# Optimization experiments

Hardware: AMD Instinct MI355X
Metric: run time of the kernel (lower is better)

The kernel has to match this reference:

```python
import jax, jax.numpy as jnp
import numpy as np

B, L, D = 4, 2048, 1024
H, KD, VD = 16, 64, 64
EPS = 1e-5


def setup_inputs() -> dict:
    key = jax.random.key(0)
    ks = jax.random.split(key, 12)
    s_in = 1.0 / np.sqrt(D)
    s_out = 1.0 / np.sqrt(H * VD)
    return {
        "queries": jax.random.normal(ks[0], (B, L, D), dtype=jnp.float32),
        "Wq": jax.random.uniform(ks[1], (D, H * KD), jnp.float32, -s_in, s_in),
        "bq": jax.random.uniform(ks[2], (H * KD,), jnp.float32, -s_in, s_in),
        "Wk": jax.random.uniform(ks[3], (D, H * KD), jnp.float32, -s_in, s_in),
        "bk": jax.random.uniform(ks[4], (H * KD,), jnp.float32, -s_in, s_in),
        "Wv": jax.random.uniform(ks[5], (D, H * VD), jnp.float32, -s_in, s_in),
        "bv": jax.random.uniform(ks[6], (H * VD,), jnp.float32, -s_in, s_in),
        "Wo": jax.random.uniform(ks[7], (H * VD, D), jnp.float32, -s_out, s_out),
        "bo": jax.random.uniform(ks[8], (D,), jnp.float32, -s_out, s_out),
        "gamma": jnp.ones((D,), jnp.float32),
        "beta": jnp.zeros((D,), jnp.float32),
    }


def reference(queries, Wq, bq, Wk, bk, Wv, bv, Wo, bo, gamma, beta):
    # QKV projections -> [B, L, H, head_dim]
    q = (queries @ Wq + bq).reshape(B, L, H, KD)
    k = (queries @ Wk + bk).reshape(B, L, H, KD)
    v = (queries @ Wv + bv).reshape(B, L, H, VD)
    # scaled dot-product attention per head: scores [B, H, Lq, Lk]
    scores = jnp.einsum("bqhd,bkhd->bhqk", q, k) / np.sqrt(KD).astype(np.float32)
    attn = jax.nn.softmax(scores, axis=-1)
    out = jnp.einsum("bhqk,bkhd->bqhd", attn, v).reshape(B, L, H * VD)
    # out projection (dropout is identity in eval), residual + LayerNorm
    res = out @ Wo + bo + queries
    mu = jnp.mean(res, axis=-1, keepdims=True)
    var = jnp.var(res, axis=-1, keepdims=True)
    return (res - mu) / jnp.sqrt(var + EPS) * gamma + beta
```

## Files before the change

### kernel.cpp

```cpp
#include <hip/hip_runtime.h>
#include <hip/hip_bf16.h>

#define BATCH 4
#define SEQ   2048
#define DIM   1024
#define NHEAD 16
#define HDIM  64
#define EPS_LN 1e-5f
#define QSCALE 0.18033688011112042f

typedef __attribute__((ext_vector_type(8))) short short8;
typedef __attribute__((ext_vector_type(4))) float f32x4;
typedef __attribute__((ext_vector_type(4))) unsigned uint32x4;

__device__ __forceinline__ unsigned short f2bf(float x) {
    __hip_bfloat16 h = __float2bfloat16(x);
    return *reinterpret_cast<unsigned short*>(&h);
}
__device__ __forceinline__ unsigned int pack2bf(float a, float b) {
    __hip_bfloat162 h = __float22bfloat162_rn(float2{a, b});
    return *reinterpret_cast<unsigned int*>(&h);
}

__device__ __forceinline__ void pl32_swap(unsigned& a, unsigned& b) {
    asm("v_permlane32_swap_b32 %0, %1" : "+v"(a), "+v"(b));
}
__device__ __forceinline__ void pl16_swap(unsigned& a, unsigned& b) {
    asm("v_permlane16_swap_b32 %0, %1" : "+v"(a), "+v"(b));
}

__device__ __forceinline__ void gl_lds16(const void* g, void* l) {
    __builtin_amdgcn_global_load_lds(
        (const __attribute__((address_space(1))) unsigned int*)g,
        (__attribute__((address_space(3))) unsigned int*)l,
        16, 0, 0);
}

__global__ __launch_bounds__(256) void prep_kernel(const float* __restrict__ W0,
                                                   const float* __restrict__ W1,
                                                   const float* __restrict__ W2,
                                                   const float* __restrict__ W3,
                                                   const float* __restrict__ queries,
                                                   unsigned short* __restrict__ Wqkvt,
                                                   unsigned short* __restrict__ Wot,
                                                   unsigned short* __restrict__ qout)
{
    const int z = blockIdx.z;
    const int t = threadIdx.x;

    if (z == 4) {
        const int nthr = 16 * 16 * 256;
        int i = (blockIdx.y * 16 + blockIdx.x) * 256 + t;
        for (int it = 0; it < (BATCH * SEQ * DIM / 4) / nthr; it++, i += nthr) {
            float4 v = ((const float4*)queries)[i];
            ushort4 u;
            u.x = f2bf(v.x); u.y = f2bf(v.y); u.z = f2bf(v.z); u.w = f2bf(v.w);
            ((ushort4*)qout)[i] = u;
        }
        return;
    }

    __shared__ float Ts[64][65];
    const float* W = (z == 0) ? W0 : (z == 1) ? W1 : (z == 2) ? W2 : W3;
    unsigned short* Wt = (z == 3) ? Wot : (Wqkvt + (size_t)z * DIM * DIM);

    const int k0 = blockIdx.y * 64, n0 = blockIdx.x * 64;
    const int lr = t >> 2, lq = t & 3;

#pragma unroll
    for (int i = 0; i < 4; i++) {
        float4 v = *(const float4*)(W + (size_t)(k0 + lr) * DIM + n0 + (lq * 4 + i) * 4);
        Ts[lr][(lq * 4 + i) * 4 + 0] = v.x;
        Ts[lr][(lq * 4 + i) * 4 + 1] = v.y;
        Ts[lr][(lq * 4 + i) * 4 + 2] = v.z;
        Ts[lr][(lq * 4 + i) * 4 + 3] = v.w;
    }
    __syncthreads();
#pragma unroll
    for (int i = 0; i < 4; i++) {
        const int c = lq * 16 + i * 4;
        ushort4 u;
        u.x = f2bf(Ts[c + 0][lr]);
        u.y = f2bf(Ts[c + 1][lr]);
        u.z = f2bf(Ts[c + 2][lr]);
        u.w = f2bf(Ts[c + 3][lr]);
        *(ushort4*)(Wt + (size_t)(n0 + lr) * DIM + k0 + c) = u;
    }
}

__global__ __launch_bounds__(256) void gemm_qkv(const unsigned short* __restrict__ A,
                                                const unsigned short* __restrict__ Bt,
                                                const float* __restrict__ bq,
                                                const float* __restrict__ bk,
                                                const float* __restrict__ bv,
                                                unsigned short* __restrict__ Qbf,
                                                unsigned short* __restrict__ Kbf,
                                                unsigned short* __restrict__ Vtb)
{
    __shared__ __attribute__((aligned(16))) unsigned short As[128 * 32];
    __shared__ __attribute__((aligned(16))) unsigned short Bs[128 * 32];

    const int tid = threadIdx.x;
    const int w = tid >> 6, lane = tid & 63;
    const int col = lane & 15, quad = lane >> 4;
    const int wm = (w >> 1) * 64, wn = (w & 1) * 64;
    const int m0 = blockIdx.y * 128, n0 = blockIdx.x * 128;

    f32x4 acc[4][4] = {};
    const int srow = tid >> 2, sc4 = tid & 3;

    for (int k0 = 0; k0 < DIM; k0 += 32) {
        __syncthreads();
#pragma unroll
        for (int it = 0; it < 2; it++) {
            gl_lds16(A  + (size_t)(m0 + srow + it * 64) * DIM + k0 + sc4 * 8,
                     (char*)As + w * 1024 + it * 4096);
            gl_lds16(Bt + (size_t)(n0 + srow + it * 64) * DIM + k0 + sc4 * 8,
                     (char*)Bs + w * 1024 + it * 4096);
        }
        __syncthreads();

        short8 af[4], bf[4];
#pragma unroll
        for (int mt = 0; mt < 4; mt++) af[mt] = *(short8*)&As[(wm + mt * 16 + col) * 32 + quad * 8];
#pragma unroll
        for (int nt = 0; nt < 4; nt++) bf[nt] = *(short8*)&Bs[(wn + nt * 16 + col) * 32 + quad * 8];

#pragma unroll
        for (int mt = 0; mt < 4; mt++)
#pragma unroll
            for (int nt = 0; nt < 4; nt++)
                acc[mt][nt] = __builtin_amdgcn_mfma_f32_16x16x32_bf16(af[mt], bf[nt], acc[mt][nt], 0, 0, 0);
    }

    const int sector = n0 >> 10;
    const float* bias = (sector == 0) ? bq : (sector == 1) ? bk : bv;

#pragma unroll
    for (int nt = 0; nt < 4; nt++) {
        const int n = n0 + wn + nt * 16 + col;
        const int nloc = n - (sector << 10);
        const float bvv = bias[nloc];
#pragma unroll
        for (int mt = 0; mt < 4; mt++) {
            const int mbase = m0 + wm + mt * 16 + quad * 4;
            if (sector == 0) {
#pragma unroll
                for (int r = 0; r < 4; r++)
                    Qbf[(size_t)(mbase + r) * DIM + nloc] = f2bf((acc[mt][nt][r] + bvv) * QSCALE);
            } else if (sector == 1) {
#pragma unroll
                for (int r = 0; r < 4; r++)
                    Kbf[(size_t)(mbase + r) * DIM + nloc] = f2bf(acc[mt][nt][r] + bvv);
            } else {
                const int h = nloc >> 6, d = nloc & 63;
                const int b = mbase >> 11, l = mbase & 2047;
                ushort4 u;
                u.x = f2bf(acc[mt][nt][0] + bvv);
                u.y = f2bf(acc[mt][nt][1] + bvv);
                u.z = f2bf(acc[mt][nt][2] + bvv);
                u.w = f2bf(acc[mt][nt][3] + bvv);
                *(ushort4*)(Vtb + ((size_t)((b * NHEAD + h) * HDIM + d)) * SEQ + l) = u;
            }
        }
    }
}

__global__ __launch_bounds__(256) void gemm_out(const unsigned short* __restrict__ A,
                                                const unsigned short* __restrict__ Bt,
                                                const float* __restrict__ bias,
                                                const float* __restrict__ resid,
                                                float* __restrict__ Cout)
{
    __shared__ __attribute__((aligned(16))) unsigned short As[128 * 32];
    __shared__ __attribute__((aligned(16))) unsigned short Bs[128 * 32];

    const int tid = threadIdx.x;
    const int w = tid >> 6, lane = tid & 63;
    const int col = lane & 15, quad = lane >> 4;
    const int wm = (w >> 1) * 64, wn = (w & 1) * 64;
    const int m0 = blockIdx.y * 128, n0 = blockIdx.x * 128;

    f32x4 acc[4][4] = {};
    const int srow = tid >> 2, sc4 = tid & 3;

    for (int k0 = 0; k0 < DIM; k0 += 32) {
        __syncthreads();
#pragma unroll
        for (int it = 0; it < 2; it++) {
            gl_lds16(A  + (size_t)(m0 + srow + it * 64) * DIM + k0 + sc4 * 8,
                     (char*)As + w * 1024 + it * 4096);
            gl_lds16(Bt + (size_t)(n0 + srow + it * 64) * DIM + k0 + sc4 * 8,
                     (char*)Bs + w * 1024 + it * 4096);
        }
        __syncthreads();

        short8 af[4], bf[4];
#pragma unroll
        for (int mt = 0; mt < 4; mt++) af[mt] = *(short8*)&As[(wm + mt * 16 + col) * 32 + quad * 8];
#pragma unroll
        for (int nt = 0; nt < 4; nt++) bf[nt] = *(short8*)&Bs[(wn + nt * 16 + col) * 32 + quad * 8];

#pragma unroll
        for (int mt = 0; mt < 4; mt++)
#pragma unroll
            for (int nt = 0; nt < 4; nt++)
                acc[mt][nt] = __builtin_amdgcn_mfma_f32_16x16x32_bf16(af[mt], bf[nt], acc[mt][nt], 0, 0, 0);
    }

#pragma unroll
    for (int nt = 0; nt < 4; nt++) {
        const int n = n0 + wn + nt * 16 + col;
        const float bvv = bias[n];
#pragma unroll
        for (int mt = 0; mt < 4; mt++) {
            const int mbase = m0 + wm + mt * 16 + quad * 4;
#pragma unroll
            for (int r = 0; r < 4; r++) {
                const size_t off = (size_t)(mbase + r) * DIM + n;
                Cout[off] = acc[mt][nt][r] + bvv + resid[off];
            }
        }
    }
}

__global__ __launch_bounds__(512) void attn_mfma(const unsigned short* __restrict__ Qb,
                                                 const unsigned short* __restrict__ Kb,
                                                 const unsigned short* __restrict__ Vt,
                                                 unsigned short* __restrict__ Ob)
{
    __shared__ __attribute__((aligned(16))) unsigned short Ks[2 * 64 * 64];
    __shared__ __attribute__((aligned(16))) unsigned short Vs[2 * 64 * 64];

    const int tid = threadIdx.x;
    const int w = tid >> 6, lane = tid & 63;
    const int col = lane & 15, quad = lane >> 4;
    const int cs  = col & 7;
    const int ca  = quad ^ cs;
    const int cb  = (quad ^ 4) ^ cs;

    const int bh  = blockIdx.x & 63;
    const int qt_ = blockIdx.x >> 6;
    const int b   = bh >> 4;
    const int h   = bh & 15;

    const int q0 = qt_ * 256 + w * 32;

    short8 qf[2][2];
#pragma unroll
    for (int qt = 0; qt < 2; qt++) {
        const size_t base = ((size_t)(b * SEQ) + q0 + qt * 16 + col) * DIM + h * HDIM + quad * 8;
        qf[qt][0] = *(const short8*)(Qb + base);
        qf[qt][1] = *(const short8*)(Qb + base + 32);
    }

    short8 onesf;
    {
        const short v = (col == 0) ? (short)0x3F80 : (short)0;
        onesf = short8{v, v, v, v, v, v, v, v};
    }

    f32x4 o[4][2] = {};
    f32x4 od[2]   = {};

    const size_t kbase0 = ((size_t)(b * SEQ)) * DIM + h * HDIM;
    const size_t vbase0 = ((size_t)((b * NHEAD + h) * HDIM)) * SEQ;

    const int lr  = lane >> 3;
    const int swc = (lane & 7) ^ lr;

    {
        const int row = w * 8 + lr;
        gl_lds16(Kb + kbase0 + (size_t)row * DIM + swc * 8, (char*)Ks + w * 1024);
        gl_lds16(Vt + vbase0 + (size_t)row * SEQ + swc * 8, (char*)Vs + w * 1024);
    }
    __syncthreads();

    for (int kt = 0; kt < SEQ / 64; kt++) {
        const int cur = kt & 1, nxt = cur ^ 1;
        const unsigned short* Ksb = Ks + cur * 4096;
        const unsigned short* Vsb = Vs + cur * 4096;

        if (kt + 1 < SEQ / 64) {
            const int row = w * 8 + lr;
            gl_lds16(Kb + kbase0 + (size_t)((kt + 1) * 64 + row) * DIM + swc * 8,
                     (char*)Ks + nxt * 8192 + w * 1024);
            gl_lds16(Vt + vbase0 + (size_t)row * SEQ + (kt + 1) * 64 + swc * 8,
                     (char*)Vs + nxt * 8192 + w * 1024);
        }

        short8 pf[2][2];
#pragma unroll
        for (int f = 0; f < 2; f++) {
            short8 kfe0 = *(short8*)&Ksb[((f * 2 + 0) * 16 + col) * 64 + ca * 8];
            short8 kfe1 = *(short8*)&Ksb[((f * 2 + 0) * 16 + col) * 64 + cb * 8];
            short8 kfo0 = *(short8*)&Ksb[((f * 2 + 1) * 16 + col) * 64 + ca * 8];
            short8 kfo1 = *(short8*)&Ksb[((f * 2 + 1) * 16 + col) * 64 + cb * 8];
#pragma unroll
            for (int qt = 0; qt < 2; qt++) {
                f32x4 se = {};
                se = __builtin_amdgcn_mfma_f32_16x16x32_bf16(kfe0, qf[qt][0], se, 0, 0, 0);
                se = __builtin_amdgcn_mfma_f32_16x16x32_bf16(kfe1, qf[qt][1], se, 0, 0, 0);
                f32x4 so = {};
                so = __builtin_amdgcn_mfma_f32_16x16x32_bf16(kfo0, qf[qt][0], so, 0, 0, 0);
                so = __builtin_amdgcn_mfma_f32_16x16x32_bf16(kfo1, qf[qt][1], so, 0, 0, 0);

                unsigned a0 = pack2bf(__builtin_amdgcn_exp2f(se[0]), __builtin_amdgcn_exp2f(se[1]));
                unsigned b0 = pack2bf(__builtin_amdgcn_exp2f(se[2]), __builtin_amdgcn_exp2f(se[3]));
                unsigned a1 = pack2bf(__builtin_amdgcn_exp2f(so[0]), __builtin_amdgcn_exp2f(so[1]));
                unsigned b1 = pack2bf(__builtin_amdgcn_exp2f(so[2]), __builtin_amdgcn_exp2f(so[3]));

                pl32_swap(a0, a1);
                pl32_swap(b0, b1);
                pl16_swap(a0, a1);
                pl16_swap(b0, b1);

                uint32x4 cv = {a0, b0, a1, b1};
                pf[qt][f] = __builtin_bit_cast(short8, cv);
            }
        }

        __builtin_amdgcn_s_setprio(1);
#pragma unroll
        for (int qt = 0; qt < 2; qt++) {
            od[qt] = __builtin_amdgcn_mfma_f32_16x16x32_bf16(onesf, pf[qt][0], od[qt], 0, 0, 0);
            od[qt] = __builtin_amdgcn_mfma_f32_16x16x32_bf16(onesf, pf[qt][1], od[qt], 0, 0, 0);
        }

#pragma unroll
        for (int mt = 0; mt < 4; mt++) {
            short8 vf0 = *(short8*)&Vsb[(mt * 16 + col) * 64 + ca * 8];
            short8 vf1 = *(short8*)&Vsb[(mt * 16 + col) * 64 + cb * 8];
#pragma unroll
            for (int qt = 0; qt < 2; qt++) {
                o[mt][qt] = __builtin_amdgcn_mfma_f32_16x16x32_bf16(vf0, pf[qt][0], o[mt][qt], 0, 0, 0);
                o[mt][qt] = __builtin_amdgcn_mfma_f32_16x16x32_bf16(vf1, pf[qt][1], o[mt][qt], 0, 0, 0);
            }
        }
        __builtin_amdgcn_s_setprio(0);

        __syncthreads();
    }

#pragma unroll
    for (int qt = 0; qt < 2; qt++) {
        const float den = __shfl(od[qt][0], col);
        const float inv = 1.f / den;
        const size_t rowoff = ((size_t)(b * SEQ) + q0 + qt * 16 + col) * DIM + h * HDIM;
#pragma unroll
        for (int mt = 0; mt < 4; mt++) {
            ushort4 u;
            u.x = f2bf(o[mt][qt][0] * inv);
            u.y = f2bf(o[mt][qt][1] * inv);
            u.z = f2bf(o[mt][qt][2] * inv);
            u.w = f2bf(o[mt][qt][3] * inv);
            *(ushort4*)(Ob + rowoff + mt * 16 + quad * 4) = u;
        }
    }
}

__global__ __launch_bounds__(256) void layernorm_kernel(float* __restrict__ res,
                                                        const float* __restrict__ gamma,
                                                        const float* __restrict__ beta)
{
    const int tid = threadIdx.x;
    const int row = blockIdx.x;
    float4 xv = ((const float4*)(res + (size_t)row * DIM))[tid];

    float s  = xv.x + xv.y + xv.z + xv.w;
    float sq = xv.x * xv.x + xv.y * xv.y + xv.z * xv.z + xv.w * xv.w;
#pragma unroll
    for (int off = 32; off; off >>= 1) {
        s  += __shfl_xor(s, off);
        sq += __shfl_xor(sq, off);
    }
    __shared__ float sm[8];
    const int w = tid >> 6, lane = tid & 63;
    if (lane == 0) { sm[w] = s; sm[4 + w] = sq; }
    __syncthreads();
    const float st  = sm[0] + sm[1] + sm[2] + sm[3];
    const float sqt = sm[4] + sm[5] + sm[6] + sm[7];
    const float mu   = st * (1.f / DIM);
    const float var  = sqt * (1.f / DIM) - mu * mu;
    const float rstd = rsqrtf(var + EPS_LN);

    float4 g  = ((const float4*)gamma)[tid];
    float4 be = ((const float4*)beta)[tid];
    float4 o;
    o.x = (xv.x - mu) * rstd * g.x + be.x;
    o.y = (xv.y - mu) * rstd * g.y + be.y;
    o.z = (xv.z - mu) * rstd * g.z + be.z;
    o.w = (xv.w - mu) * rstd * g.w + be.w;
    ((float4*)(res + (size_t)row * DIM))[tid] = o;
}

extern "C" void kernel_launch(void* const* d_in, const int* in_sizes, int n_in,
                              void* d_out, int out_size, void* d_ws, size_t ws_size,
                              hipStream_t stream)
{
    const float* queries = (const float*)d_in[0];
    const float* Wq = (const float*)d_in[1];
    const float* bq = (const float*)d_in[2];
    const float* Wk = (const float*)d_in[3];
    const float* bk = (const float*)d_in[4];
    const float* Wv = (const float*)d_in[5];
    const float* bv = (const float*)d_in[6];
    const float* Wo = (const float*)d_in[7];
    const float* bo = (const float*)d_in[8];
    const float* gamma = (const float*)d_in[9];
    const float* beta  = (const float*)d_in[10];
    float* outp = (float*)d_out;

    const int M = BATCH * SEQ;
    const size_t BUF = (size_t)M * DIM;
    const size_t WSZ = (size_t)DIM * DIM;

    unsigned short* w0  = (unsigned short*)d_ws;
    unsigned short* qin = w0;
    unsigned short* Qbf = w0 + BUF;
    unsigned short* Kbf = w0 + 2 * BUF;
    unsigned short* Vtb = w0 + 3 * BUF;
    unsigned short* Wqkvt = w0 + 4 * BUF;
    unsigned short* Wot   = Wqkvt + 3 * WSZ;
    unsigned short* Obf = qin;

    dim3 blk(256);

    dim3 pgrid(DIM / 64, DIM / 64, 5);
    prep_kernel<<<pgrid, blk, 0, stream>>>(Wq, Wk, Wv, Wo, queries, Wqkvt, Wot, qin);

    dim3 qkvgrid(3 * DIM / 128, M / 128);
    gemm_qkv<<<qkvgrid, blk, 0, stream>>>(qin, Wqkvt, bq, bk, bv, Qbf, Kbf, Vtb);

    attn_mfma<<<BATCH * NHEAD * (SEQ / 256), dim3(512), 0, stream>>>(Qbf, Kbf, Vtb, Obf);

    dim3 ogrid(DIM / 128, M / 128);
    gemm_out<<<ogrid, blk, 0, stream>>>(Obf, Wot, bo, queries, outp);

    layernorm_kernel<<<M, blk, 0, stream>>>(outp, gamma, beta);
}
```

Before: 305.5 us.

## Split attention key tiles across warp pairs and reduce partial outputs in LDS

Each block now covers 128 queries instead of 256. Its 8 warps form 4 query groups × 2 key halves: each warp computes scores and P·V for half of each 64-key tile. The two partial outputs and denominators are then combined through shared memory (reusing the K/V buffers) before normalisation and the store. This doubles the grid to 1024 blocks for better CU occupancy and load balance, at the cost of twice as many K/V tile loads per query and an extra LDS reduction at the end.

New measurement: 308.1 us. No clear change (+0.8%).

```diff
diff --git a/kernel.cpp b/kernel.cpp
--- a/kernel.cpp
+++ b/kernel.cpp
@@ -231,9 +231,11 @@
 {
     __shared__ __attribute__((aligned(16))) unsigned short Ks[2 * 64 * 64];
     __shared__ __attribute__((aligned(16))) unsigned short Vs[2 * 64 * 64];
+    __shared__ float DsX[128];
 
     const int tid = threadIdx.x;
     const int w = tid >> 6, lane = tid & 63;
+    const int qw = w & 3, kw = w >> 2;
     const int col = lane & 15, quad = lane >> 4;
     const int cs  = col & 7;
     const int ca  = quad ^ cs;
@@ -244,7 +246,7 @@
     const int b   = bh >> 4;
     const int h   = bh & 15;
 
-    const int q0 = qt_ * 256 + w * 32;
+    const int q0 = qt_ * 128 + qw * 32;
 
     short8 qf[2][2];
 #pragma unroll
@@ -289,13 +291,13 @@
                      (char*)Vs + nxt * 8192 + w * 1024);
         }
 
-        short8 pf[2][2];
-#pragma unroll
-        for (int f = 0; f < 2; f++) {
-            short8 kfe0 = *(short8*)&Ksb[((f * 2 + 0) * 16 + col) * 64 + ca * 8];
-            short8 kfe1 = *(short8*)&Ksb[((f * 2 + 0) * 16 + col) * 64 + cb * 8];
-            short8 kfo0 = *(short8*)&Ksb[((f * 2 + 1) * 16 + col) * 64 + ca * 8];
-            short8 kfo1 = *(short8*)&Ksb[((f * 2 + 1) * 16 + col) * 64 + cb * 8];
+        short8 pf[2];
+        {
+            const int nte = kw * 2 + 0, nto = kw * 2 + 1;
+            short8 kfe0 = *(short8*)&Ksb[(nte * 16 + col) * 64 + ca * 8];
+            short8 kfe1 = *(short8*)&Ksb[(nte * 16 + col) * 64 + cb * 8];
+            short8 kfo0 = *(short8*)&Ksb[(nto * 16 + col) * 64 + ca * 8];
+            short8 kfo1 = *(short8*)&Ksb[(nto * 16 + col) * 64 + cb * 8];
 #pragma unroll
             for (int qt = 0; qt < 2; qt++) {
                 f32x4 se = {};
@@ -316,45 +318,57 @@
                 pl16_swap(b0, b1);
 
                 uint32x4 cv = {a0, b0, a1, b1};
-                pf[qt][f] = __builtin_bit_cast(short8, cv);
+                pf[qt] = __builtin_bit_cast(short8, cv);
             }
         }
 
         __builtin_amdgcn_s_setprio(1);
 #pragma unroll
+        for (int qt = 0; qt < 2; qt++)
+            od[qt] = __builtin_amdgcn_mfma_f32_16x16x32_bf16(onesf, pf[qt], od[qt], 0, 0, 0);
+
+#pragma unroll
+        for (int mt = 0; mt < 4; mt++) {
+            short8 vf = *(short8*)&Vsb[(mt * 16 + col) * 64 + (kw ? cb : ca) * 8];
+#pragma unroll
+            for (int qt = 0; qt < 2; qt++)
+                o[mt][qt] = __builtin_amdgcn_mfma_f32_16x16x32_bf16(vf, pf[qt], o[mt][qt], 0, 0, 0);
+        }
+        __builtin_amdgcn_s_setprio(0);
+
+        __syncthreads();
+    }
+
+    float4* xbuf = (qw & 2) ? (float4*)Vs : (float4*)Ks;
+    const int xbase = (qw & 1) * 512;
+    if (kw == 1) {
+#pragma unroll
+        for (int mt = 0; mt < 4; mt++)
+#pragma unroll
+            for (int qt = 0; qt < 2; qt++)
+                xbuf[xbase + (mt * 2 + qt) * 64 + lane] = __builtin_bit_cast(float4, o[mt][qt]);
+        if (quad == 0) {
+            DsX[(qw * 2 + 0) * 16 + col] = od[0][0];
+            DsX[(qw * 2 + 1) * 16 + col] = od[1][0];
+        }
+    }
+    __syncthreads();
+    if (kw == 0) {
+#pragma unroll
         for (int qt = 0; qt < 2; qt++) {
-            od[qt] = __builtin_amdgcn_mfma_f32_16x16x32_bf16(onesf, pf[qt][0], od[qt], 0, 0, 0);
-            od[qt] = __builtin_amdgcn_mfma_f32_16x16x32_bf16(onesf, pf[qt][1], od[qt], 0, 0, 0);
-        }
-
-#pragma unroll
-        for (int mt = 0; mt < 4; mt++) {
-            short8 vf0 = *(short8*)&Vsb[(mt * 16 + col) * 64 + ca * 8];
-            short8 vf1 = *(short8*)&Vsb[(mt * 16 + col) * 64 + cb * 8];
-#pragma unroll
-            for (int qt = 0; qt < 2; qt++) {
-                o[mt][qt] = __builtin_amdgcn_mfma_f32_16x16x32_bf16(vf0, pf[qt][0], o[mt][qt], 0, 0, 0);
-                o[mt][qt] = __builtin_amdgcn_mfma_f32_16x16x32_bf16(vf1, pf[qt][1], o[mt][qt], 0, 0, 0);
+            const float den = __shfl(od[qt][0], col) + DsX[(qw * 2 + qt) * 16 + col];
+            const float inv = 1.f / den;
+            const size_t rowoff = ((size_t)(b * SEQ) + q0 + qt * 16 + col) * DIM + h * HDIM;
+#pragma unroll
+            for (int mt = 0; mt < 4; mt++) {
+                const float4 p = xbuf[xbase + (mt * 2 + qt) * 64 + lane];
+                ushort4 u;
+                u.x = f2bf((o[mt][qt][0] + p.x) * inv);
+                u.y = f2bf((o[mt][qt][1] + p.y) * inv);
+                u.z = f2bf((o[mt][qt][2] + p.z) * inv);
+                u.w = f2bf((o[mt][qt][3] + p.w) * inv);
+                *(ushort4*)(Ob + rowoff + mt * 16 + quad * 4) = u;
             }
-        }
-        __builtin_amdgcn_s_setprio(0);
-
-        __syncthreads();
-    }
-
-#pragma unroll
-    for (int qt = 0; qt < 2; qt++) {
-        const float den = __shfl(od[qt][0], col);
-        const float inv = 1.f / den;
-        const size_t rowoff = ((size_t)(b * SEQ) + q0 + qt * 16 + col) * DIM + h * HDIM;
-#pragma unroll
-        for (int mt = 0; mt < 4; mt++) {
-            ushort4 u;
-            u.x = f2bf(o[mt][qt][0] * inv);
-            u.y = f2bf(o[mt][qt][1] * inv);
-            u.z = f2bf(o[mt][qt][2] * inv);
-            u.w = f2bf(o[mt][qt][3] * inv);
-            *(ushort4*)(Ob + rowoff + mt * 16 + quad * 4) = u;
         }
     }
 }
@@ -432,7 +446,7 @@
     dim3 qkvgrid(3 * DIM / 128, M / 128);
     gemm_qkv<<<qkvgrid, blk, 0, stream>>>(qin, Wqkvt, bq, bk, bv, Qbf, Kbf, Vtb);
 
-    attn_mfma<<<BATCH * NHEAD * (SEQ / 256), dim3(512), 0, stream>>>(Qbf, Kbf, Vtb, Obf);
+    attn_mfma<<<BATCH * NHEAD * (SEQ / 128), dim3(512), 0, stream>>>(Qbf, Kbf, Vtb, Obf);
 
     dim3 ogrid(DIM / 128, M / 128);
     gemm_out<<<ogrid, blk, 0, stream>>>(Obf, Wot, bo, queries, outp);
```

## Double KV tile to 128 keys per iteration and interleave QK and PV per 32-key group

Applied to the files above, without the earlier changes.

The attention kernel now loads 128 keys per iteration, with double-buffered K and V tiles of twice the previous size, so the loop runs half as many times and needs half as many block barriers. Inside the iteration, each 32-key group computes its scores, exponentiates them and immediately feeds the PV and denominator MFMAs. Before, all scores for the tile were computed first and the PV MFMAs ran afterwards. This is meant to cut synchronization overhead and improve MFMA and exp interleaving, at the cost of double the LDS (64KB per block), which may lower occupancy.

Measured after the change: 293.0 us. 4.1% less time.

```diff
diff --git a/kernel.cpp b/kernel.cpp
--- a/kernel.cpp
+++ b/kernel.cpp
@@ -229,8 +229,8 @@
                                                  const unsigned short* __restrict__ Vt,
                                                  unsigned short* __restrict__ Ob)
 {
-    __shared__ __attribute__((aligned(16))) unsigned short Ks[2 * 64 * 64];
-    __shared__ __attribute__((aligned(16))) unsigned short Vs[2 * 64 * 64];
+    __shared__ __attribute__((aligned(16))) unsigned short Ks[2 * 128 * 64];
+    __shared__ __attribute__((aligned(16))) unsigned short Vs[2 * 2 * 64 * 64];
 
     const int tid = threadIdx.x;
     const int w = tid >> 6, lane = tid & 63;
@@ -269,33 +269,48 @@
     const int lr  = lane >> 3;
     const int swc = (lane & 7) ^ lr;
 
-    {
+#pragma unroll
+    for (int it = 0; it < 2; it++) {
+        const int row = it * 64 + w * 8 + lr;
+        gl_lds16(Kb + kbase0 + (size_t)row * DIM + swc * 8,
+                 (char*)Ks + it * 8192 + w * 1024);
+    }
+#pragma unroll
+    for (int hv = 0; hv < 2; hv++) {
         const int row = w * 8 + lr;
-        gl_lds16(Kb + kbase0 + (size_t)row * DIM + swc * 8, (char*)Ks + w * 1024);
-        gl_lds16(Vt + vbase0 + (size_t)row * SEQ + swc * 8, (char*)Vs + w * 1024);
+        gl_lds16(Vt + vbase0 + (size_t)row * SEQ + hv * 64 + swc * 8,
+                 (char*)Vs + hv * 8192 + w * 1024);
     }
     __syncthreads();
 
-    for (int kt = 0; kt < SEQ / 64; kt++) {
+    for (int kt = 0; kt < SEQ / 128; kt++) {
         const int cur = kt & 1, nxt = cur ^ 1;
-        const unsigned short* Ksb = Ks + cur * 4096;
-        const unsigned short* Vsb = Vs + cur * 4096;
-
-        if (kt + 1 < SEQ / 64) {
-            const int row = w * 8 + lr;
-            gl_lds16(Kb + kbase0 + (size_t)((kt + 1) * 64 + row) * DIM + swc * 8,
-                     (char*)Ks + nxt * 8192 + w * 1024);
-            gl_lds16(Vt + vbase0 + (size_t)row * SEQ + (kt + 1) * 64 + swc * 8,
-                     (char*)Vs + nxt * 8192 + w * 1024);
-        }
-
-        short8 pf[2][2];
-#pragma unroll
-        for (int f = 0; f < 2; f++) {
-            short8 kfe0 = *(short8*)&Ksb[((f * 2 + 0) * 16 + col) * 64 + ca * 8];
-            short8 kfe1 = *(short8*)&Ksb[((f * 2 + 0) * 16 + col) * 64 + cb * 8];
-            short8 kfo0 = *(short8*)&Ksb[((f * 2 + 1) * 16 + col) * 64 + ca * 8];
-            short8 kfo1 = *(short8*)&Ksb[((f * 2 + 1) * 16 + col) * 64 + cb * 8];
+        const unsigned short* Ksb = Ks + cur * 8192;
+        const unsigned short* Vsb = Vs + cur * 8192;
+
+        if (kt + 1 < SEQ / 128) {
+#pragma unroll
+            for (int it = 0; it < 2; it++) {
+                const int row = it * 64 + w * 8 + lr;
+                gl_lds16(Kb + kbase0 + (size_t)((kt + 1) * 128 + row) * DIM + swc * 8,
+                         (char*)Ks + nxt * 16384 + it * 8192 + w * 1024);
+            }
+#pragma unroll
+            for (int hv = 0; hv < 2; hv++) {
+                const int row = w * 8 + lr;
+                gl_lds16(Vt + vbase0 + (size_t)row * SEQ + (kt + 1) * 128 + hv * 64 + swc * 8,
+                         (char*)Vs + nxt * 16384 + hv * 8192 + w * 1024);
+            }
+        }
+
+#pragma unroll
+        for (int g = 0; g < 4; g++) {
+            short8 kfe0 = *(short8*)&Ksb[((g * 2 + 0) * 16 + col) * 64 + ca * 8];
+            short8 kfe1 = *(short8*)&Ksb[((g * 2 + 0) * 16 + col) * 64 + cb * 8];
+            short8 kfo0 = *(short8*)&Ksb[((g * 2 + 1) * 16 + col) * 64 + ca * 8];
+            short8 kfo1 = *(short8*)&Ksb[((g * 2 + 1) * 16 + col) * 64 + cb * 8];
+
+            short8 pf[2];
 #pragma unroll
             for (int qt = 0; qt < 2; qt++) {
                 f32x4 se = {};
@@ -316,28 +331,25 @@
                 pl16_swap(b0, b1);
 
                 uint32x4 cv = {a0, b0, a1, b1};
-                pf[qt][f] = __builtin_bit_cast(short8, cv);
-            }
-        }
-
-        __builtin_amdgcn_s_setprio(1);
-#pragma unroll
-        for (int qt = 0; qt < 2; qt++) {
-            od[qt] = __builtin_amdgcn_mfma_f32_16x16x32_bf16(onesf, pf[qt][0], od[qt], 0, 0, 0);
-            od[qt] = __builtin_amdgcn_mfma_f32_16x16x32_bf16(onesf, pf[qt][1], od[qt], 0, 0, 0);
-        }
-
-#pragma unroll
-        for (int mt = 0; mt < 4; mt++) {
-            short8 vf0 = *(short8*)&Vsb[(mt * 16 + col) * 64 + ca * 8];
-            short8 vf1 = *(short8*)&Vsb[(mt * 16 + col) * 64 + cb * 8];
-#pragma unroll
-            for (int qt = 0; qt < 2; qt++) {
-                o[mt][qt] = __builtin_amdgcn_mfma_f32_16x16x32_bf16(vf0, pf[qt][0], o[mt][qt], 0, 0, 0);
-                o[mt][qt] = __builtin_amdgcn_mfma_f32_16x16x32_bf16(vf1, pf[qt][1], o[mt][qt], 0, 0, 0);
-            }
-        }
-        __builtin_amdgcn_s_setprio(0);
+                pf[qt] = __builtin_bit_cast(short8, cv);
+            }
+
+            __builtin_amdgcn_s_setprio(1);
+#pragma unroll
+            for (int qt = 0; qt < 2; qt++)
+                od[qt] = __builtin_amdgcn_mfma_f32_16x16x32_bf16(onesf, pf[qt], od[qt], 0, 0, 0);
+
+            const int hv = g >> 1;
+            const int coff = (g & 1) ? cb : ca;
+#pragma unroll
+            for (int mt = 0; mt < 4; mt++) {
+                short8 vf = *(short8*)&Vsb[hv * 4096 + (mt * 16 + col) * 64 + coff * 8];
+#pragma unroll
+                for (int qt = 0; qt < 2; qt++)
+                    o[mt][qt] = __builtin_amdgcn_mfma_f32_16x16x32_bf16(vf, pf[qt], o[mt][qt], 0, 0, 0);
+            }
+            __builtin_amdgcn_s_setprio(0);
+        }
 
         __syncthreads();
     }
```
